# Kernel optimization log

Measured on AMD Instinct MI355X. Metric: run time of the kernel, lower is better.

The kernel has to match this reference:

```python
import jax, jax.numpy as jnp
import numpy as np
import math

N_HEAD = 16
HEAD_DIM = 64
N_EMBD = N_HEAD * HEAD_DIM  # 1024


def _alibi_slopes(n_heads):
    def pow2(n):
        start = 2.0 ** (-2.0 ** (-(math.log2(n) - 3)))
        return [start * (start ** i) for i in range(n)]
    if n_heads & (n_heads - 1) == 0:
        s = pow2(n_heads)
    else:
        cp2 = 2 ** math.floor(math.log2(n_heads))
        s = pow2(cp2)
        extra_base = 2.0 ** (-2.0 ** (-(math.log2(2 * cp2) - 3)))
        s += [extra_base * (extra_base ** i) for i in range(n_heads - cp2)]
        s = s[:n_heads]
    return jnp.asarray(np.array(s, dtype=np.float32))


def setup_inputs() -> dict:
    key = jax.random.key(0)
    k1, k2, k3, k4 = jax.random.split(key, 4)
    B, T = 2, 2048
    x = jax.random.normal(k1, (B, T, N_EMBD), dtype=jnp.float32)
    # c_attn weight for q,k (use_v=True -> 2*n_embd outputs), no bias
    W_attn = jax.random.normal(k2, (N_EMBD, 2 * N_EMBD), dtype=jnp.float32) * 0.02
    v_tmp = jax.random.normal(k3, (N_HEAD, N_HEAD), dtype=jnp.float32) * 0.02
    proj_tmp = jax.random.normal(k4, (N_HEAD, N_HEAD), dtype=jnp.float32) * 0.02
    return {"x": x, "W_attn": W_attn, "v_tmp": v_tmp, "proj_tmp": proj_tmp}


def reference(x, W_attn, v_tmp, proj_tmp):
    B, T, C = x.shape
    H, D = N_HEAD, HEAD_DIM
    scale = 1.0 / math.sqrt(D)

    qk = x @ W_attn  # (B,T,2C)
    q, k = qk[..., :C], qk[..., C:]
    q = q.reshape(B, T, H, D).transpose(0, 2, 1, 3)  # (B,H,T,D)
    k = k.reshape(B, T, H, D).transpose(0, 2, 1, 3)

    # V via Kronecker-lifted matrix: x @ kron(v_tmp, I_D)
    # block structure => mix head channels: out[...,j,d] = sum_i x[...,i,d]*v_tmp[i,j]
    xh = x.reshape(B, T, H, D)
    v = jnp.einsum('btid,ij->btjd', xh, v_tmp)  # (B,T,H,D)

    scores = jnp.einsum('bhqd,bhkd->bhqk', q, k) * scale  # (B,H,T,T)

    # ALiBi bias + causal mask
    pos = jnp.arange(T, dtype=jnp.float32)
    rel = pos[None, :] - pos[:, None]  # (T,T), mem - ctx
    slopes = _alibi_slopes(H)
    bias = slopes[:, None, None] * rel[None, :, :]
    causal = pos[None, :] <= pos[:, None]
    bias = jnp.where(causal[None, :, :], bias, -jnp.inf)
    scores = scores + bias[None]

    att = jax.nn.softmax(scores, axis=-1)
    y = jnp.einsum('bhqk,bkhd->bqhd', att, v)  # (B,T,H,D)

    # output proj via kron(proj_tmp, I_D).T: out[...,i,d] = sum_j y[...,j,d]*proj_tmp[i,j]
    y = jnp.einsum('btjd,ij->btid', y, proj_tmp)
    return y.reshape(B, T, C)
```

## Files before the change

### kernel.cpp

```cpp
#include <hip/hip_runtime.h>

typedef __attribute__((ext_vector_type(8))) __bf16 bf16x8;
typedef __attribute__((ext_vector_type(8))) unsigned short u16x8;
typedef __attribute__((ext_vector_type(4))) float f32x4;
typedef __attribute__((ext_vector_type(4))) unsigned int u32x4;

#define LOG2E 1.4426950408889634f

#define GLDS16(gp, lp)                                                \
  __builtin_amdgcn_global_load_lds(                                   \
      (const __attribute__((address_space(1))) void*)(gp),            \
      (__attribute__((address_space(3))) void*)(lp), 16, 0, 0)

__device__ __forceinline__ unsigned short f2b(float f) {
  return __builtin_bit_cast(unsigned short, (__bf16)f);
}
__device__ __forceinline__ float b2f(unsigned short h) {
  return __uint_as_float(((unsigned)h) << 16);
}
__device__ __forceinline__ unsigned cvt_pk(float a, float b) {
  unsigned r;
  asm("v_cvt_pk_bf16_f32 %0, %1, %2" : "=v"(r) : "v"(a), "v"(b));
  return r;
}
__device__ __forceinline__ void swap32(unsigned& a, unsigned& b) {
  asm("v_permlane32_swap_b32 %0, %1" : "+v"(a), "+v"(b));
}
__device__ __forceinline__ void swap16(unsigned& a, unsigned& b) {
  asm("v_permlane16_swap_b32 %0, %1" : "+v"(a), "+v"(b));
}

__global__ __launch_bounds__(256) void k_pre(const float* __restrict__ x,
                                             const float* __restrict__ vt,
                                             const float* __restrict__ W,
                                             unsigned short* __restrict__ xb,
                                             unsigned short* __restrict__ vb,
                                             unsigned short* __restrict__ Wt) {
  if (blockIdx.x < 1024) {
    __shared__ float s_vt[256];
    s_vt[threadIdx.x] = vt[threadIdx.x];
    __syncthreads();
    int g = blockIdx.x * 256 + threadIdx.x;
    int bt = g >> 6, d = g & 63;
    const float* xp = x + (size_t)bt * 1024 + d;
    float xi[16];
#pragma unroll
    for (int i = 0; i < 16; ++i) xi[i] = xp[i * 64];
#pragma unroll
    for (int i = 0; i < 16; ++i) xb[(size_t)bt * 1024 + i * 64 + d] = f2b(xi[i]);
#pragma unroll
    for (int j = 0; j < 16; ++j) {
      float s = 0.f;
#pragma unroll
      for (int i = 0; i < 16; ++i) s += xi[i] * s_vt[i * 16 + j];
      vb[(size_t)bt * 1024 + j * 64 + d] = f2b(s);
    }
  } else {
    __shared__ unsigned short tile[64][65];
    int id2 = blockIdx.x - 1024;
    int n0 = (id2 & 31) * 64;
    int k0 = (id2 >> 5) * 64;
    int tx = threadIdx.x & 63, ty = threadIdx.x >> 6;
#pragma unroll
    for (int r = 0; r < 16; ++r) {
      int kk = ty * 16 + r;
      tile[kk][tx] = f2b(W[(size_t)(k0 + kk) * 2048 + n0 + tx]);
    }
    __syncthreads();
#pragma unroll
    for (int r = 0; r < 16; ++r) {
      int nn = ty * 16 + r;
      Wt[(size_t)(n0 + nn) * 1024 + k0 + tx] = tile[tx][nn];
    }
  }
}

__global__ __launch_bounds__(256) void k_mid(const unsigned short* __restrict__ A,
                                             const unsigned short* __restrict__ Bt,
                                             unsigned short* __restrict__ C,
                                             const unsigned short* __restrict__ vb,
                                             unsigned short* __restrict__ Vt) {
  if (blockIdx.x < 512) {
    __shared__ unsigned short As[128 * 32];
    __shared__ unsigned short Bs[128 * 32];
    const int K = 1024;
    int m0 = (blockIdx.x & 31) * 128;
    int n0 = (blockIdx.x >> 5) * 128;
    int tid = threadIdx.x;
    int w = tid >> 6, lane = tid & 63;
    int lq = lane & 15, lk8 = (lane >> 4) * 8;
    int wr = (w >> 1) * 64, wc = (w & 1) * 64;
    f32x4 acc[4][4];
#pragma unroll
    for (int i = 0; i < 4; ++i)
#pragma unroll
      for (int j = 0; j < 4; ++j)
#pragma unroll
        for (int r = 0; r < 4; ++r) acc[i][j][r] = 0.f;

    for (int kk = 0; kk < K; kk += 32) {
      __syncthreads();
#pragma unroll
      for (int i = 0; i < 2; ++i) {
        int c = tid + 256 * i;
        int row = c >> 2, col = (c & 3) * 8;
        GLDS16(A + (size_t)(m0 + row) * K + kk + col, As + c * 8);
        GLDS16(Bt + (size_t)(n0 + row) * K + kk + col, Bs + c * 8);
      }
      __syncthreads();
      bf16x8 af[4], bf[4];
#pragma unroll
      for (int i = 0; i < 4; ++i) af[i] = *(const bf16x8*)(As + (wr + i * 16 + lq) * 32 + lk8);
#pragma unroll
      for (int j = 0; j < 4; ++j) bf[j] = *(const bf16x8*)(Bs + (wc + j * 16 + lq) * 32 + lk8);
#pragma unroll
      for (int i = 0; i < 4; ++i)
#pragma unroll
        for (int j = 0; j < 4; ++j)
          acc[i][j] = __builtin_amdgcn_mfma_f32_16x16x32_bf16(af[i], bf[j], acc[i][j], 0, 0, 0);
    }
#pragma unroll
    for (int i = 0; i < 4; ++i)
#pragma unroll
      for (int j = 0; j < 4; ++j)
#pragma unroll
        for (int r = 0; r < 4; ++r) {
          int m = m0 + wr + i * 16 + (lane >> 4) * 4 + r;
          int n = n0 + wc + j * 16 + lq;
          C[(size_t)m * 2048 + n] = f2b(acc[i][j][r]);
        }
  } else {
    __shared__ unsigned short tile[64][65];
    int id2 = blockIdx.x - 512;
    int t0 = (id2 & 31) * 64;
    int c0 = ((id2 >> 5) & 15) * 64;
    int b = id2 >> 9;
    int tx = threadIdx.x & 63, ty = threadIdx.x >> 6;
#pragma unroll
    for (int r = 0; r < 16; ++r) {
      int tt = ty * 16 + r;
      tile[tt][tx] = vb[((size_t)b * 2048 + t0 + tt) * 1024 + c0 + tx];
    }
    __syncthreads();
#pragma unroll
    for (int r = 0; r < 16; ++r) {
      int cc = ty * 16 + r;
      Vt[((size_t)b * 1024 + c0 + cc) * 2048 + t0 + tx] = tile[tx][cc];
    }
  }
}

__global__ __launch_bounds__(256, 4) void k_flash(const unsigned short* __restrict__ qkb,
                                                  const unsigned short* __restrict__ Vt,
                                                  unsigned short* __restrict__ y) {
  __shared__ unsigned short Ks[2][2][64 * 32];
  __shared__ unsigned short Vs[2][2][64 * 32];
  int id = blockIdx.x;
  int xcd = id & 7, s = id >> 3;
  int grp = xcd + 8 * (s & 3);
  int qt = 31 - (s >> 2);
  int hd = grp & 15, b = grp >> 4;
  int tid = threadIdx.x;
  int w = tid >> 6, lane = tid & 63;
  int quad = lane >> 4, lq = lane & 15, lk8 = quad * 8;
  int xk8 = (quad ^ ((lq >> 1) & 3)) * 8;
  int rs = tid >> 2;
  int csw = ((tid & 3) ^ ((tid >> 3) & 3)) * 8;
  const size_t rowb = (size_t)b * 2048;
  const size_t vrow = ((size_t)b * 1024 + hd * 64 + rs) * 2048 + csw;
  const size_t krow = ((rowb + rs) << 11) + 1024 + hd * 64 + csw;

  float slope = exp2f(-0.5f * (float)(hd + 1));
  const float c1 = 0.125f * LOG2E;
  const float c2 = slope * LOG2E;
  const float SHIFT = 16.0f;

  bf16x8 ones;
#pragma unroll
  for (int i = 0; i < 8; ++i) ones[i] = (__bf16)1.0f;

  int q0 = qt * 64;
  int qr_l = q0 + w * 16 + lq;
  bf16x8 qf0 = *(const bf16x8*)(qkb + ((rowb + qr_l) << 11) + hd * 64 + lk8);
  bf16x8 qf1 = *(const bf16x8*)(qkb + ((rowb + qr_l) << 11) + hd * 64 + 32 + lk8);

  float base_b[4][4];
#pragma unroll
  for (int s4 = 0; s4 < 4; ++s4)
#pragma unroll
    for (int r = 0; r < 4; ++r)
      base_b[s4][r] = c2 * (float)(s4 * 16 + quad * 4 + r - qr_l) - SHIFT;

  f32x4 o[4], o4;
#pragma unroll
  for (int r = 0; r < 4; ++r) o4[r] = 0.f;
#pragma unroll
  for (int jj = 0; jj < 4; ++jj)
#pragma unroll
    for (int r = 0; r < 4; ++r) o[jj][r] = 0.f;

  GLDS16(qkb + krow,      &Ks[0][0][rs * 32 + (tid & 3) * 8]);
  GLDS16(qkb + krow + 32, &Ks[0][1][rs * 32 + (tid & 3) * 8]);
  GLDS16(Vt + vrow,       &Vs[0][0][rs * 32 + (tid & 3) * 8]);
  GLDS16(Vt + vrow + 32,  &Vs[0][1][rs * 32 + (tid & 3) * 8]);
  __syncthreads();
  int cur = 0;

#pragma unroll 1
  for (int kt = 0; kt <= qt; ++kt) {
    int k0 = kt * 64;
    if (kt < qt) {
      size_t koff = (size_t)(k0 + 64);
      int nxt = cur ^ 1;
      GLDS16(qkb + krow + (koff << 11),      &Ks[nxt][0][rs * 32 + (tid & 3) * 8]);
      GLDS16(qkb + krow + (koff << 11) + 32, &Ks[nxt][1][rs * 32 + (tid & 3) * 8]);
      GLDS16(Vt + vrow + koff,               &Vs[nxt][0][rs * 32 + (tid & 3) * 8]);
      GLDS16(Vt + vrow + koff + 32,          &Vs[nxt][1][rs * 32 + (tid & 3) * 8]);
    }
    bf16x8 kc[4][2];
#pragma unroll
    for (int s4 = 0; s4 < 4; ++s4) {
      u16x8 t0 = *(const u16x8*)(&Ks[cur][0][(s4 * 16 + lq) * 32 + xk8]);
      u16x8 t1 = *(const u16x8*)(&Ks[cur][1][(s4 * 16 + lq) * 32 + xk8]);
      kc[s4][0] = __builtin_bit_cast(bf16x8, t0);
      kc[s4][1] = __builtin_bit_cast(bf16x8, t1);
    }
    f32x4 S[4];
#pragma unroll
    for (int s4 = 0; s4 < 4; ++s4) {
      f32x4 a;
#pragma unroll
      for (int r = 0; r < 4; ++r) a[r] = 0.f;
      a = __builtin_amdgcn_mfma_f32_16x16x32_bf16(kc[s4][0], qf0, a, 0, 0, 0);
      a = __builtin_amdgcn_mfma_f32_16x16x32_bf16(kc[s4][1], qf1, a, 0, 0, 0);
      S[s4] = a;
    }
    float bk = c2 * (float)k0;
    float p[4][4];
    if (kt == qt) {
#pragma unroll
      for (int s4 = 0; s4 < 4; ++s4)
#pragma unroll
        for (int r = 0; r < 4; ++r) {
          float v = S[s4][r] * c1 + (base_b[s4][r] + bk);
          v = (k0 + s4 * 16 + quad * 4 + r <= qr_l) ? v : -1e30f;
          p[s4][r] = exp2f(v);
        }
    } else {
#pragma unroll
      for (int s4 = 0; s4 < 4; ++s4)
#pragma unroll
        for (int r = 0; r < 4; ++r) {
          float v = S[s4][r] * c1 + (base_b[s4][r] + bk);
          p[s4][r] = exp2f(v);
        }
    }
    unsigned pk[4][2];
#pragma unroll
    for (int s4 = 0; s4 < 4; ++s4) {
      pk[s4][0] = cvt_pk(p[s4][0], p[s4][1]);
      pk[s4][1] = cvt_pk(p[s4][2], p[s4][3]);
    }
    bf16x8 pf[2];
#pragma unroll
    for (int c = 0; c < 2; ++c) {
      unsigned a0 = pk[2 * c][0], b0 = pk[2 * c + 1][0];
      swap32(a0, b0); swap16(a0, b0);
      unsigned a1 = pk[2 * c][1], b1 = pk[2 * c + 1][1];
      swap32(a1, b1); swap16(a1, b1);
      u32x4 t; t[0] = a0; t[1] = a1; t[2] = b0; t[3] = b1;
      pf[c] = __builtin_bit_cast(bf16x8, t);
    }
    o4 = __builtin_amdgcn_mfma_f32_16x16x32_bf16(ones, pf[0], o4, 0, 0, 0);
    o4 = __builtin_amdgcn_mfma_f32_16x16x32_bf16(ones, pf[1], o4, 0, 0, 0);
#pragma unroll
    for (int jj = 0; jj < 4; ++jj) {
      u16x8 v0 = *(const u16x8*)(&Vs[cur][0][(jj * 16 + lq) * 32 + xk8]);
      u16x8 v1 = *(const u16x8*)(&Vs[cur][1][(jj * 16 + lq) * 32 + xk8]);
      bf16x8 vf0 = __builtin_bit_cast(bf16x8, v0);
      bf16x8 vf1 = __builtin_bit_cast(bf16x8, v1);
      o[jj] = __builtin_amdgcn_mfma_f32_16x16x32_bf16(vf0, pf[0], o[jj], 0, 0, 0);
      o[jj] = __builtin_amdgcn_mfma_f32_16x16x32_bf16(vf1, pf[1], o[jj], 0, 0, 0);
    }
    if (kt < qt) {
      __syncthreads();
      cur ^= 1;
    }
  }
  float inv = 1.0f / o4[0];
  size_t base = ((rowb + qr_l) << 10) + hd * 64 + quad * 4;
#pragma unroll
  for (int jj = 0; jj < 4; ++jj) {
    ushort4 pk4;
    pk4.x = f2b(o[jj][0] * inv);
    pk4.y = f2b(o[jj][1] * inv);
    pk4.z = f2b(o[jj][2] * inv);
    pk4.w = f2b(o[jj][3] * inv);
    *(ushort4*)(y + base + jj * 16) = pk4;
  }
}

__global__ __launch_bounds__(256) void k_proj(const unsigned short* __restrict__ yb,
                                              const float* __restrict__ pt,
                                              float* __restrict__ out) {
  __shared__ float s_pt[256];
  s_pt[threadIdx.x] = pt[threadIdx.x];
  __syncthreads();
  int g = blockIdx.x * 256 + threadIdx.x;
  int bt = g >> 6, d = g & 63;
  float yj[16];
#pragma unroll
  for (int j = 0; j < 16; ++j) yj[j] = b2f(yb[(size_t)bt * 1024 + j * 64 + d]);
#pragma unroll
  for (int i = 0; i < 16; ++i) {
    float s = 0.f;
#pragma unroll
    for (int j = 0; j < 16; ++j) s += yj[j] * s_pt[i * 16 + j];
    out[(size_t)bt * 1024 + i * 64 + d] = s;
  }
}

extern "C" void kernel_launch(void* const* d_in, const int* in_sizes, int n_in,
                              void* d_out, int out_size, void* d_ws, size_t ws_size,
                              hipStream_t stream) {
  const float* x  = (const float*)d_in[0];
  const float* W  = (const float*)d_in[1];
  const float* vt = (const float*)d_in[2];
  const float* pt = (const float*)d_in[3];
  float* out = (float*)d_out;

  char* ws = (char*)d_ws;
  unsigned short* xb  = (unsigned short*)(ws);
  unsigned short* Wt  = (unsigned short*)(ws + (8u  << 20));
  unsigned short* qkb = (unsigned short*)(ws + (12u << 20));
  unsigned short* vb  = (unsigned short*)(ws + (28u << 20));
  unsigned short* Vtr = (unsigned short*)(ws + (36u << 20));
  unsigned short* yb  = xb;

  k_pre  <<<1536, 256, 0, stream>>>(x, vt, W, xb, vb, Wt);
  k_mid  <<<1536, 256, 0, stream>>>(xb, Wt, qkb, vb, Vtr);
  k_flash<<<1024, 256, 0, stream>>>(qkb, Vtr, yb);
  k_proj <<<1024, 256, 0, stream>>>(yb, pt, out);
}
```

Before: 153.3 us.

## Split flash-attention warps into 2x2 query/key tiles with LDS partial-sum reduction

Each of the four waves previously handled 16 query rows against all 64 keys of a tile. Now the waves form a 2x2 grid: each handles 32 query rows and half of the key tile, so each wave reads half the K and V fragments from LDS and reuses them across two query sub-tiles. The two key-half partial outputs and row sums are combined at the end through LDS, with an extra barrier. s_setprio hints are also placed around the MFMA sections. The trade-offs are more accumulator registers, a bit more ALiBi bias arithmetic, and an epilogue reduction.

```diff
diff --git a/kernel.cpp b/kernel.cpp
--- a/kernel.cpp
+++ b/kernel.cpp
@@ -164,6 +164,7 @@
   int w = tid >> 6, lane = tid & 63;
   int quad = lane >> 4, lq = lane & 15, lk8 = quad * 8;
   int xk8 = (quad ^ ((lq >> 1) & 3)) * 8;
+  int qh = w >> 1, kh = w & 1;
   int rs = tid >> 2;
   int csw = ((tid & 3) ^ ((tid >> 3) & 3)) * 8;
   const size_t rowb = (size_t)b * 2048;
@@ -173,6 +174,7 @@
   float slope = exp2f(-0.5f * (float)(hd + 1));
   const float c1 = 0.125f * LOG2E;
   const float c2 = slope * LOG2E;
+  const float c16 = 16.0f * c2;
   const float SHIFT = 16.0f;
 
   bf16x8 ones;
@@ -180,24 +182,29 @@
   for (int i = 0; i < 8; ++i) ones[i] = (__bf16)1.0f;
 
   int q0 = qt * 64;
-  int qr_l = q0 + w * 16 + lq;
-  bf16x8 qf0 = *(const bf16x8*)(qkb + ((rowb + qr_l) << 11) + hd * 64 + lk8);
-  bf16x8 qf1 = *(const bf16x8*)(qkb + ((rowb + qr_l) << 11) + hd * 64 + 32 + lk8);
-
-  float base_b[4][4];
-#pragma unroll
-  for (int s4 = 0; s4 < 4; ++s4)
-#pragma unroll
-    for (int r = 0; r < 4; ++r)
-      base_b[s4][r] = c2 * (float)(s4 * 16 + quad * 4 + r - qr_l) - SHIFT;
-
-  f32x4 o[4], o4;
-#pragma unroll
-  for (int r = 0; r < 4; ++r) o4[r] = 0.f;
+  int qrow = q0 + qh * 32;
+  bf16x8 qf[2][2];
+#pragma unroll
+  for (int qs2 = 0; qs2 < 2; ++qs2) {
+    int qg = qrow + qs2 * 16 + lq;
+    qf[qs2][0] = *(const bf16x8*)(qkb + ((rowb + qg) << 11) + hd * 64 + lk8);
+    qf[qs2][1] = *(const bf16x8*)(qkb + ((rowb + qg) << 11) + hd * 64 + 32 + lk8);
+  }
+  int kq0 = kh * 32 + quad * 4 - qrow - lq;
+  float base0[4];
+#pragma unroll
+  for (int r = 0; r < 4; ++r) base0[r] = c2 * (float)(kq0 + r) - SHIFT;
+
+  f32x4 o[4][2];
+  f32x4 o4[2];
+#pragma unroll
+  for (int r = 0; r < 4; ++r) { o4[0][r] = 0.f; o4[1][r] = 0.f; }
 #pragma unroll
   for (int jj = 0; jj < 4; ++jj)
 #pragma unroll
-    for (int r = 0; r < 4; ++r) o[jj][r] = 0.f;
+    for (int qs2 = 0; qs2 < 2; ++qs2)
+#pragma unroll
+      for (int r = 0; r < 4; ++r) o[jj][qs2][r] = 0.f;
 
   GLDS16(qkb + krow,      &Ks[0][0][rs * 32 + (tid & 3) * 8]);
   GLDS16(qkb + krow + 32, &Ks[0][1][rs * 32 + (tid & 3) * 8]);
@@ -217,86 +224,125 @@
       GLDS16(Vt + vrow + koff,               &Vs[nxt][0][rs * 32 + (tid & 3) * 8]);
       GLDS16(Vt + vrow + koff + 32,          &Vs[nxt][1][rs * 32 + (tid & 3) * 8]);
     }
-    bf16x8 kc[4][2];
-#pragma unroll
-    for (int s4 = 0; s4 < 4; ++s4) {
-      u16x8 t0 = *(const u16x8*)(&Ks[cur][0][(s4 * 16 + lq) * 32 + xk8]);
-      u16x8 t1 = *(const u16x8*)(&Ks[cur][1][(s4 * 16 + lq) * 32 + xk8]);
-      kc[s4][0] = __builtin_bit_cast(bf16x8, t0);
-      kc[s4][1] = __builtin_bit_cast(bf16x8, t1);
-    }
-    f32x4 S[4];
-#pragma unroll
-    for (int s4 = 0; s4 < 4; ++s4) {
-      f32x4 a;
-#pragma unroll
-      for (int r = 0; r < 4; ++r) a[r] = 0.f;
-      a = __builtin_amdgcn_mfma_f32_16x16x32_bf16(kc[s4][0], qf0, a, 0, 0, 0);
-      a = __builtin_amdgcn_mfma_f32_16x16x32_bf16(kc[s4][1], qf1, a, 0, 0, 0);
-      S[s4] = a;
-    }
+    bf16x8 kc[2][2];
+#pragma unroll
+    for (int ks2 = 0; ks2 < 2; ++ks2) {
+      u16x8 t0 = *(const u16x8*)(&Ks[cur][0][(kh * 32 + ks2 * 16 + lq) * 32 + xk8]);
+      u16x8 t1 = *(const u16x8*)(&Ks[cur][1][(kh * 32 + ks2 * 16 + lq) * 32 + xk8]);
+      kc[ks2][0] = __builtin_bit_cast(bf16x8, t0);
+      kc[ks2][1] = __builtin_bit_cast(bf16x8, t1);
+    }
+    __builtin_amdgcn_s_setprio(1);
+    f32x4 S[2][2];
+#pragma unroll
+    for (int ks2 = 0; ks2 < 2; ++ks2)
+#pragma unroll
+      for (int qs2 = 0; qs2 < 2; ++qs2) {
+        f32x4 a;
+#pragma unroll
+        for (int r = 0; r < 4; ++r) a[r] = 0.f;
+        a = __builtin_amdgcn_mfma_f32_16x16x32_bf16(kc[ks2][0], qf[qs2][0], a, 0, 0, 0);
+        a = __builtin_amdgcn_mfma_f32_16x16x32_bf16(kc[ks2][1], qf[qs2][1], a, 0, 0, 0);
+        S[ks2][qs2] = a;
+      }
+    __builtin_amdgcn_s_setprio(0);
     float bk = c2 * (float)k0;
-    float p[4][4];
+    float p[2][2][4];
     if (kt == qt) {
 #pragma unroll
-      for (int s4 = 0; s4 < 4; ++s4)
-#pragma unroll
-        for (int r = 0; r < 4; ++r) {
-          float v = S[s4][r] * c1 + (base_b[s4][r] + bk);
-          v = (k0 + s4 * 16 + quad * 4 + r <= qr_l) ? v : -1e30f;
-          p[s4][r] = exp2f(v);
-        }
+      for (int ks2 = 0; ks2 < 2; ++ks2)
+#pragma unroll
+        for (int qs2 = 0; qs2 < 2; ++qs2)
+#pragma unroll
+          for (int r = 0; r < 4; ++r) {
+            float v = S[ks2][qs2][r] * c1 + (base0[r] + bk + c16 * (float)(ks2 - qs2));
+            v = (k0 + kq0 + (ks2 - qs2) * 16 + r <= 0) ? v : -1e30f;
+            p[ks2][qs2][r] = exp2f(v);
+          }
     } else {
 #pragma unroll
-      for (int s4 = 0; s4 < 4; ++s4)
-#pragma unroll
-        for (int r = 0; r < 4; ++r) {
-          float v = S[s4][r] * c1 + (base_b[s4][r] + bk);
-          p[s4][r] = exp2f(v);
-        }
-    }
-    unsigned pk[4][2];
-#pragma unroll
-    for (int s4 = 0; s4 < 4; ++s4) {
-      pk[s4][0] = cvt_pk(p[s4][0], p[s4][1]);
-      pk[s4][1] = cvt_pk(p[s4][2], p[s4][3]);
-    }
+      for (int ks2 = 0; ks2 < 2; ++ks2)
+#pragma unroll
+        for (int qs2 = 0; qs2 < 2; ++qs2)
+#pragma unroll
+          for (int r = 0; r < 4; ++r) {
+            float v = S[ks2][qs2][r] * c1 + (base0[r] + bk + c16 * (float)(ks2 - qs2));
+            p[ks2][qs2][r] = exp2f(v);
+          }
+    }
+    unsigned pk[2][2][2];
+#pragma unroll
+    for (int ks2 = 0; ks2 < 2; ++ks2)
+#pragma unroll
+      for (int qs2 = 0; qs2 < 2; ++qs2) {
+        pk[ks2][qs2][0] = cvt_pk(p[ks2][qs2][0], p[ks2][qs2][1]);
+        pk[ks2][qs2][1] = cvt_pk(p[ks2][qs2][2], p[ks2][qs2][3]);
+      }
     bf16x8 pf[2];
 #pragma unroll
-    for (int c = 0; c < 2; ++c) {
-      unsigned a0 = pk[2 * c][0], b0 = pk[2 * c + 1][0];
+    for (int qs2 = 0; qs2 < 2; ++qs2) {
+      unsigned a0 = pk[0][qs2][0], b0 = pk[1][qs2][0];
       swap32(a0, b0); swap16(a0, b0);
-      unsigned a1 = pk[2 * c][1], b1 = pk[2 * c + 1][1];
+      unsigned a1 = pk[0][qs2][1], b1 = pk[1][qs2][1];
       swap32(a1, b1); swap16(a1, b1);
       u32x4 t; t[0] = a0; t[1] = a1; t[2] = b0; t[3] = b1;
-      pf[c] = __builtin_bit_cast(bf16x8, t);
-    }
-    o4 = __builtin_amdgcn_mfma_f32_16x16x32_bf16(ones, pf[0], o4, 0, 0, 0);
-    o4 = __builtin_amdgcn_mfma_f32_16x16x32_bf16(ones, pf[1], o4, 0, 0, 0);
+      pf[qs2] = __builtin_bit_cast(bf16x8, t);
+    }
+    __builtin_amdgcn_s_setprio(1);
+    o4[0] = __builtin_amdgcn_mfma_f32_16x16x32_bf16(ones, pf[0], o4[0], 0, 0, 0);
+    o4[1] = __builtin_amdgcn_mfma_f32_16x16x32_bf16(ones, pf[1], o4[1], 0, 0, 0);
 #pragma unroll
     for (int jj = 0; jj < 4; ++jj) {
-      u16x8 v0 = *(const u16x8*)(&Vs[cur][0][(jj * 16 + lq) * 32 + xk8]);
-      u16x8 v1 = *(const u16x8*)(&Vs[cur][1][(jj * 16 + lq) * 32 + xk8]);
-      bf16x8 vf0 = __builtin_bit_cast(bf16x8, v0);
-      bf16x8 vf1 = __builtin_bit_cast(bf16x8, v1);
-      o[jj] = __builtin_amdgcn_mfma_f32_16x16x32_bf16(vf0, pf[0], o[jj], 0, 0, 0);
-      o[jj] = __builtin_amdgcn_mfma_f32_16x16x32_bf16(vf1, pf[1], o[jj], 0, 0, 0);
-    }
+      u16x8 v0 = *(const u16x8*)(&Vs[cur][kh][(jj * 16 + lq) * 32 + xk8]);
+      bf16x8 vf = __builtin_bit_cast(bf16x8, v0);
+      o[jj][0] = __builtin_amdgcn_mfma_f32_16x16x32_bf16(vf, pf[0], o[jj][0], 0, 0, 0);
+      o[jj][1] = __builtin_amdgcn_mfma_f32_16x16x32_bf16(vf, pf[1], o[jj][1], 0, 0, 0);
+    }
+    __builtin_amdgcn_s_setprio(0);
     if (kt < qt) {
       __syncthreads();
       cur ^= 1;
     }
   }
-  float inv = 1.0f / o4[0];
-  size_t base = ((rowb + qr_l) << 10) + hd * 64 + quad * 4;
-#pragma unroll
-  for (int jj = 0; jj < 4; ++jj) {
-    ushort4 pk4;
-    pk4.x = f2b(o[jj][0] * inv);
-    pk4.y = f2b(o[jj][1] * inv);
-    pk4.z = f2b(o[jj][2] * inv);
-    pk4.w = f2b(o[jj][3] * inv);
-    *(ushort4*)(y + base + jj * 16) = pk4;
+
+  __syncthreads();
+  float* red0 = (float*)&Ks[0][0][0];
+  float* red1 = (float*)&Vs[0][0][0];
+  float* red = (qh ? red1 : red0) + lane * 36;
+  if (kh == 1) {
+#pragma unroll
+    for (int jj = 0; jj < 4; ++jj)
+#pragma unroll
+      for (int qs2 = 0; qs2 < 2; ++qs2)
+#pragma unroll
+        for (int r = 0; r < 4; ++r) red[(jj * 2 + qs2) * 4 + r] = o[jj][qs2][r];
+    red[32] = o4[0][0];
+    red[33] = o4[1][0];
+  }
+  __syncthreads();
+  if (kh == 0) {
+#pragma unroll
+    for (int jj = 0; jj < 4; ++jj)
+#pragma unroll
+      for (int qs2 = 0; qs2 < 2; ++qs2)
+#pragma unroll
+        for (int r = 0; r < 4; ++r) o[jj][qs2][r] += red[(jj * 2 + qs2) * 4 + r];
+    float inv0 = 1.0f / (o4[0][0] + red[32]);
+    float inv1 = 1.0f / (o4[1][0] + red[33]);
+#pragma unroll
+    for (int qs2 = 0; qs2 < 2; ++qs2) {
+      float inv = qs2 ? inv1 : inv0;
+      size_t base = ((rowb + qrow + qs2 * 16 + lq) << 10) + hd * 64 + quad * 4;
+#pragma unroll
+      for (int jj = 0; jj < 4; ++jj) {
+        ushort4 pk4;
+        pk4.x = f2b(o[jj][qs2][0] * inv);
+        pk4.y = f2b(o[jj][qs2][1] * inv);
+        pk4.z = f2b(o[jj][qs2][2] * inv);
+        pk4.w = f2b(o[jj][qs2][3] * inv);
+        *(ushort4*)(y + base + jj * 16) = pk4;
+      }
+    }
   }
 }
 
```

Measured after the change: 151.2 us. No clear change (-1.4%).
